# Kernel tuning notes

Measured on AMD Instinct MI355X. Metric: run time of the kernel, lower is better.

The kernel has to match this reference:

```python
import jax, jax.numpy as jnp
import numpy as np

E = 128; H = 8; DK = 16; FFH = 512; NL = 6
DEPOT = 20; CUST = 500; N = DEPOT + CUST
B = 32; M = N; L = 40; CLIP = 10.0; EPS = 1e-5


def _heads(x):
    b, n, _ = x.shape
    return x.reshape(b, n, H, DK).transpose(0, 2, 1, 3)  # (b,H,n,dk)


def _mha(q, k, v, mask3=None):
    s = jnp.einsum('bhnd,bhmd->bhnm', q, k) / jnp.sqrt(jnp.float32(DK))
    if mask3 is not None:
        s = s + mask3[:, None, :, :]
    w = jax.nn.softmax(s, axis=-1)
    o = jnp.einsum('bhnm,bhmd->bhnd', w, v)
    return o.transpose(0, 2, 1, 3).reshape(q.shape[0], q.shape[2], H * DK)


def _inorm(x, g, b):  # InstanceNorm1d over the node axis, per (batch, channel)
    mu = x.mean(axis=1, keepdims=True)
    var = x.var(axis=1, keepdims=True)
    return (x - mu) / jnp.sqrt(var + EPS) * g + b


def setup_inputs() -> dict:
    key = jax.random.key(0)
    ks = jax.random.split(key, 30)
    rn = lambda k, s, sc=0.05: (jax.random.normal(k, s, dtype=jnp.float32) * sc)
    inp = {
        'depot_feats': jax.random.normal(ks[0], (B, DEPOT, 4), dtype=jnp.float32),
        'customer_feats': jax.random.normal(ks[1], (B, CUST, 3), dtype=jnp.float32),
        'mask': jnp.zeros((B, M, N), dtype=jnp.float32),
        'load': jax.random.uniform(ks[2], (B, M), dtype=jnp.float32),
        'current_node': jax.random.randint(ks[3], (B, M), 0, N),
        'subtour_nodes': jax.random.randint(ks[4], (B, M, L), 0, N),
        'subtour_len': jax.random.randint(ks[5], (B, M), 0, L),
        'selected': jax.random.randint(ks[6], (B, M, 4), 0, N),
        # encoder embedding layers
        'enc_dep_W': rn(ks[7], (E, 4)), 'enc_dep_b': rn(ks[8], (E,)),
        'enc_cus_W': rn(ks[9], (E, 3)), 'enc_cus_b': rn(ks[10], (E,)),
        # stacked encoder-layer params
        'Wq': rn(ks[11], (NL, E, E)), 'Wk': rn(ks[12], (NL, E, E)),
        'Wv': rn(ks[13], (NL, E, E)),
        'Wc': rn(ks[14], (NL, E, E)), 'Wc_b': rn(ks[15], (NL, E)),
        'n1_g': jnp.ones((NL, E), jnp.float32), 'n1_b': jnp.zeros((NL, E), jnp.float32),
        'ffW1': rn(ks[16], (NL, FFH, E)), 'ffb1': rn(ks[17], (NL, FFH)),
        'ffW2': rn(ks[18], (NL, E, FFH)), 'ffb2': rn(ks[19], (NL, E)),
        'n2_g': jnp.ones((NL, E), jnp.float32), 'n2_b': jnp.zeros((NL, E), jnp.float32),
        # decoder params
        'dec_Wq_loc': rn(ks[20], (E, 2 * E)),
        'dec_Wq_rout': rn(ks[21], (E, 2 * E + 1)),
        'dec_Wk': rn(ks[22], (E, E)), 'dec_Wv': rn(ks[23], (E, E)),
        'dec_Wc': rn(ks[24], (E, E)), 'dec_Wc_b': rn(ks[25], (E,)),
    }
    return inp


def reference(depot_feats, customer_feats, mask, load,
              enc_dep_W, enc_dep_b, enc_cus_W, enc_cus_b,
              Wq, Wk, Wv, Wc, Wc_b, n1_g, n1_b,
              ffW1, ffb1, ffW2, ffb2, n2_g, n2_b,
              dec_Wq_loc, dec_Wq_rout, dec_Wk, dec_Wv, dec_Wc, dec_Wc_b,
              current_node, subtour_nodes, subtour_len, selected):
    # ---- Encoder ----
    dep = depot_feats @ enc_dep_W.T + enc_dep_b
    cus = customer_feats @ enc_cus_W.T + enc_cus_b
    x = jnp.concatenate([dep, cus], axis=1)  # (B,N,E)
    for i in range(NL):
        q = _heads(x @ Wq[i].T); k = _heads(x @ Wk[i].T); v = _heads(x @ Wv[i].T)
        mh = _mha(q, k, v) @ Wc[i].T + Wc_b[i]
        x1 = _inorm(x + mh, n1_g[i], n1_b[i])
        ff = jax.nn.relu(x1 @ ffW1[i].T + ffb1[i]) @ ffW2[i].T + ffb2[i]
        x = _inorm(x1 + ff, n2_g[i], n2_b[i])
    encoded = x  # (B,N,E)

    # ---- set_k_v ----
    k_d = _heads(encoded @ dec_Wk.T)
    v_d = _heads(encoded @ dec_Wv.T)

    # ---- Decoder forward (current_node present, last_hh not None branch) ----
    enc_mean = encoded.mean(axis=1, keepdims=True)  # (B,1,E)
    enc_mean = jnp.broadcast_to(enc_mean, (B, M, E))
    b_idx = jnp.arange(B)[:, None]
    last_emb = encoded[b_idx, current_node]  # (B,M,E) gather of current node
    input_cat = jnp.concatenate([last_emb, enc_mean, load[:, :, None]], axis=2)
    q_routing = input_cat @ dec_Wq_rout.T  # (B,M,E)

    # subtour gather + masked mean pool
    bb = jnp.arange(B)[:, None, None]
    sub_embs = encoded[bb, subtour_nodes]  # (B,M,L,E)
    pos = jnp.arange(L)[None, None, :]
    valid = pos < subtour_len[:, :, None]
    is_cust = subtour_nodes >= DEPOT
    fm = (valid & is_cust).astype(jnp.float32)  # (B,M,L)
    sub_sum = jnp.einsum('bmle,bml->bme', sub_embs, fm)
    cnt = jnp.clip(fm.sum(axis=2, keepdims=True), 1.0, None)
    sub_mean = sub_sum / cnt
    q_location = jnp.concatenate([last_emb, sub_mean], axis=2) @ dec_Wq_loc.T

    # conditional query blend
    last_node = selected[:, :, -2] < DEPOT
    node = current_node < DEPOT
    flag = ((~last_node) & node).astype(jnp.float32)[:, :, None]  # (B,M,1)
    final_q = q_location * flag + q_routing * (1.0 - flag)

    q = _heads(final_q)  # (B,H,M,dk)
    attn = _mha(q, k_d, v_d, mask3=mask)  # (B,M,H*dk)
    score = attn @ dec_Wc.T + dec_Wc_b  # (B,M,E)
    score_nodes = jnp.einsum('bme,bne->bmn', score, encoded)
    score_scaled = score_nodes / jnp.sqrt(jnp.float32(E))
    score_masked = CLIP * jnp.tanh(score_scaled) + mask
    prob = jax.nn.softmax(score_masked, axis=2)
    return prob
```

## Files before the change

kernel.cpp:

```cpp
#include <hip/hip_runtime.h>
#include <hip/hip_bf16.h>

#define BB 32
#define NN 520
#define MM 520
#define EE 128
#define HH 8
#define DKK 16
#define FFH_ 512
#define NL_ 6
#define DEPOT_ 20
#define LL 40

typedef short short8 __attribute__((ext_vector_type(8)));
typedef short bshort4 __attribute__((ext_vector_type(4)));
typedef float floatx4 __attribute__((ext_vector_type(4)));

__device__ __forceinline__ unsigned short f2b(float x) {
    unsigned int u = __float_as_uint(x);
    return (unsigned short)((u + 0x7fffu + ((u >> 16) & 1u)) >> 16);
}
__device__ __forceinline__ float b2f_(unsigned short h) {
    return __uint_as_float(((unsigned int)h) << 16);
}

__global__ __launch_bounds__(256) void embed_k(
    const float* __restrict__ dep, const float* __restrict__ cus,
    const float* __restrict__ Wd, const float* __restrict__ bd,
    const float* __restrict__ Wc3, const float* __restrict__ bc,
    float* __restrict__ x)
{
    int idx = blockIdx.x * 256 + threadIdx.x;
    int e = idx & 127;
    int bn = idx >> 7;
    int n = bn % NN;
    int b = bn / NN;
    float a;
    if (n < DEPOT_) {
        a = bd[e];
        const float* f = dep + ((size_t)(b * DEPOT_ + n)) * 4;
        #pragma unroll
        for (int j = 0; j < 4; j++) a += f[j] * Wd[e * 4 + j];
    } else {
        a = bc[e];
        const float* f = cus + ((size_t)(b * 500 + (n - DEPOT_))) * 3;
        #pragma unroll
        for (int j = 0; j < 3; j++) a += f[j] * Wc3[e * 3 + j];
    }
    x[idx] = a;
}

#define WLS 196608
#define WDEC 1179648
#define WTOT 1277952
__global__ __launch_bounds__(256) void wconv_k(
    const float* __restrict__ Wq, const float* __restrict__ Wk, const float* __restrict__ Wv,
    const float* __restrict__ Wc, const float* __restrict__ fW1, const float* __restrict__ fW2,
    const float* __restrict__ dWk, const float* __restrict__ dWv, const float* __restrict__ dWc,
    const float* __restrict__ Wql, const float* __restrict__ Wqr,
    unsigned short* __restrict__ WH, unsigned short* __restrict__ WL)
{
    int idx = blockIdx.x * 256 + threadIdx.x;
    if (idx >= WTOT) return;
    const float* src;
    if (idx < WDEC) {
        int i = idx / WLS, r = idx % WLS;
        if (r < 49152) {
            int row = r >> 7, col = r & 127;
            const float* w = row < 128 ? Wq : (row < 256 ? Wk : Wv);
            src = w + (size_t)i * 16384 + (size_t)(row & 127) * 128 + col;
        } else if (r < 65536) {
            src = Wc + (size_t)i * 16384 + (r - 49152);
        } else if (r < 131072) {
            src = fW1 + (size_t)i * 65536 + (r - 65536);
        } else {
            src = fW2 + (size_t)i * 65536 + (r - 131072);
        }
    } else {
        int r = idx - WDEC;
        if (r < 32768) {
            int row = r >> 7, col = r & 127;
            src = (row < 128 ? dWk : dWv) + (size_t)(row & 127) * 128 + col;
        } else if (r < 49152) {
            src = dWc + (r - 32768);
        } else {
            int rr = r - 49152;
            int row = rr >> 7, col = rr & 127;
            if (row < 128)      src = Wqr + (size_t)row * 257 + col;
            else if (row < 256) src = Wql + (size_t)(row - 128) * 256 + col;
            else                src = Wql + (size_t)(row - 256) * 256 + 128 + col;
        }
    }
    float v = *src;
    unsigned short h = f2b(v);
    WH[idx] = h;
    WL[idx] = f2b(v - b2f_(h));
}

#define AP 40
__global__ __launch_bounds__(256) void gemm_pc_k(
    const float* __restrict__ A, int lda,
    const unsigned short* __restrict__ WH, const unsigned short* __restrict__ WL, int ldw,
    const float* __restrict__ bias,
    float* __restrict__ C, int ldc,
    int K, int relu)
{
    __shared__ __align__(16) unsigned short Ah[128][AP];
    __shared__ __align__(16) unsigned short Al[128][AP];
    __shared__ __align__(16) unsigned short Bh[64][AP];
    __shared__ __align__(16) unsigned short Bl[64][AP];

    int t = threadIdx.x;
    int w = t >> 6, lane = t & 63;
    int frow = lane & 15, fq = lane >> 4;
    int n0 = blockIdx.x * 64, m0 = blockIdx.y * 128;

    int arow = t & 127, ahalf = (t >> 7) * 16;
    int brow = t & 63,  bq    = (t >> 6) * 8;

    floatx4 acc[2][4];
    #pragma unroll
    for (int i = 0; i < 2; i++)
        #pragma unroll
        for (int j = 0; j < 4; j++)
            acc[i][j] = (floatx4){0.0f, 0.0f, 0.0f, 0.0f};

    for (int k0 = 0; k0 < K; k0 += 32) {
        {
            const float* Ap = A + (size_t)(m0 + arow) * lda + k0 + ahalf;
            float vr[16];
            #pragma unroll
            for (int j = 0; j < 4; j++) {
                float4 v = ((const float4*)Ap)[j];
                vr[j * 4 + 0] = v.x; vr[j * 4 + 1] = v.y;
                vr[j * 4 + 2] = v.z; vr[j * 4 + 3] = v.w;
            }
            short8 hv0, hv1, lv0, lv1;
            #pragma unroll
            for (int j = 0; j < 8; j++) {
                unsigned short h = f2b(vr[j]);
                hv0[j] = (short)h;
                lv0[j] = (short)f2b(vr[j] - b2f_(h));
            }
            #pragma unroll
            for (int j = 0; j < 8; j++) {
                unsigned short h = f2b(vr[8 + j]);
                hv1[j] = (short)h;
                lv1[j] = (short)f2b(vr[8 + j] - b2f_(h));
            }
            *((short8*)&Ah[arow][ahalf])     = hv0;
            *((short8*)&Ah[arow][ahalf + 8]) = hv1;
            *((short8*)&Al[arow][ahalf])     = lv0;
            *((short8*)&Al[arow][ahalf + 8]) = lv1;
        }
        {
            size_t wo = (size_t)(n0 + brow) * ldw + k0 + bq;
            *((short8*)&Bh[brow][bq]) = *((const short8*)(WH + wo));
            *((short8*)&Bl[brow][bq]) = *((const short8*)(WL + wo));
        }
        __syncthreads();

        short8 ah0 = *((const short8*)&Ah[w * 32 + frow][fq * 8]);
        short8 ah1 = *((const short8*)&Ah[w * 32 + 16 + frow][fq * 8]);
        short8 al0 = *((const short8*)&Al[w * 32 + frow][fq * 8]);
        short8 al1 = *((const short8*)&Al[w * 32 + 16 + frow][fq * 8]);
        #pragma unroll
        for (int nt = 0; nt < 4; nt++) {
            short8 bh = *((const short8*)&Bh[nt * 16 + frow][fq * 8]);
            short8 bl = *((const short8*)&Bl[nt * 16 + frow][fq * 8]);
            acc[0][nt] = __builtin_amdgcn_mfma_f32_16x16x32_bf16(ah0, bh, acc[0][nt], 0, 0, 0);
            acc[1][nt] = __builtin_amdgcn_mfma_f32_16x16x32_bf16(ah1, bh, acc[1][nt], 0, 0, 0);
            acc[0][nt] = __builtin_amdgcn_mfma_f32_16x16x32_bf16(ah0, bl, acc[0][nt], 0, 0, 0);
            acc[1][nt] = __builtin_amdgcn_mfma_f32_16x16x32_bf16(ah1, bl, acc[1][nt], 0, 0, 0);
            acc[0][nt] = __builtin_amdgcn_mfma_f32_16x16x32_bf16(al0, bh, acc[0][nt], 0, 0, 0);
            acc[1][nt] = __builtin_amdgcn_mfma_f32_16x16x32_bf16(al1, bh, acc[1][nt], 0, 0, 0);
        }
        __syncthreads();
    }

    #pragma unroll
    for (int nt = 0; nt < 4; nt++) {
        int col = n0 + nt * 16 + frow;
        float bv = bias ? bias[col] : 0.0f;
        #pragma unroll
        for (int mt = 0; mt < 2; mt++) {
            int rbase = m0 + w * 32 + mt * 16 + fq * 4;
            #pragma unroll
            for (int r = 0; r < 4; r++) {
                float v = acc[mt][nt][r] + bv;
                if (relu) v = fmaxf(v, 0.0f);
                C[(size_t)(rbase + r) * ldc + col] = v;
            }
        }
    }
}

__global__ __launch_bounds__(256) void gemm_qkv3_k(
    const float* __restrict__ A, int lda,
    const unsigned short* __restrict__ WH, const unsigned short* __restrict__ WL, int ldw,
    float* __restrict__ C0, float* __restrict__ C1, float* __restrict__ C2,
    int ldc, int K, int pack)
{
    __shared__ __align__(16) unsigned short Ah[128][AP];
    __shared__ __align__(16) unsigned short Al[128][AP];
    __shared__ __align__(16) unsigned short Bh[64][AP];
    __shared__ __align__(16) unsigned short Bl[64][AP];

    int t = threadIdx.x;
    int w = t >> 6, lane = t & 63;
    int frow = lane & 15, fq = lane >> 4;
    int nb = blockIdx.x;
    int which = nb >> 1;
    float* C = which == 0 ? C0 : (which == 1 ? C1 : C2);
    int n0w = nb * 64;
    int n0c = (nb & 1) * 64;
    int m0 = blockIdx.y * 128;

    int arow = t & 127, ahalf = (t >> 7) * 16;
    int brow = t & 63,  bq    = (t >> 6) * 8;

    floatx4 acc[2][4];
    #pragma unroll
    for (int i = 0; i < 2; i++)
        #pragma unroll
        for (int j = 0; j < 4; j++)
            acc[i][j] = (floatx4){0.0f, 0.0f, 0.0f, 0.0f};

    for (int k0 = 0; k0 < K; k0 += 32) {
        {
            const float* Ap = A + (size_t)(m0 + arow) * lda + k0 + ahalf;
            float vr[16];
            #pragma unroll
            for (int j = 0; j < 4; j++) {
                float4 v = ((const float4*)Ap)[j];
                vr[j * 4 + 0] = v.x; vr[j * 4 + 1] = v.y;
                vr[j * 4 + 2] = v.z; vr[j * 4 + 3] = v.w;
            }
            short8 hv0, hv1, lv0, lv1;
            #pragma unroll
            for (int j = 0; j < 8; j++) {
                unsigned short h = f2b(vr[j]);
                hv0[j] = (short)h;
                lv0[j] = (short)f2b(vr[j] - b2f_(h));
            }
            #pragma unroll
            for (int j = 0; j < 8; j++) {
                unsigned short h = f2b(vr[8 + j]);
                hv1[j] = (short)h;
                lv1[j] = (short)f2b(vr[8 + j] - b2f_(h));
            }
            *((short8*)&Ah[arow][ahalf])     = hv0;
            *((short8*)&Ah[arow][ahalf + 8]) = hv1;
            *((short8*)&Al[arow][ahalf])     = lv0;
            *((short8*)&Al[arow][ahalf + 8]) = lv1;
        }
        {
            size_t wo = (size_t)(n0w + brow) * ldw + k0 + bq;
            *((short8*)&Bh[brow][bq]) = *((const short8*)(WH + wo));
            *((short8*)&Bl[brow][bq]) = *((const short8*)(WL + wo));
        }
        __syncthreads();

        short8 ah0 = *((const short8*)&Ah[w * 32 + frow][fq * 8]);
        short8 ah1 = *((const short8*)&Ah[w * 32 + 16 + frow][fq * 8]);
        short8 al0 = *((const short8*)&Al[w * 32 + frow][fq * 8]);
        short8 al1 = *((const short8*)&Al[w * 32 + 16 + frow][fq * 8]);
        #pragma unroll
        for (int nt = 0; nt < 4; nt++) {
            short8 bh = *((const short8*)&Bh[nt * 16 + frow][fq * 8]);
            short8 bl = *((const short8*)&Bl[nt * 16 + frow][fq * 8]);
            acc[0][nt] = __builtin_amdgcn_mfma_f32_16x16x32_bf16(ah0, bh, acc[0][nt], 0, 0, 0);
            acc[1][nt] = __builtin_amdgcn_mfma_f32_16x16x32_bf16(ah1, bh, acc[1][nt], 0, 0, 0);
            acc[0][nt] = __builtin_amdgcn_mfma_f32_16x16x32_bf16(ah0, bl, acc[0][nt], 0, 0, 0);
            acc[1][nt] = __builtin_amdgcn_mfma_f32_16x16x32_bf16(ah1, bl, acc[1][nt], 0, 0, 0);
            acc[0][nt] = __builtin_amdgcn_mfma_f32_16x16x32_bf16(al0, bh, acc[0][nt], 0, 0, 0);
            acc[1][nt] = __builtin_amdgcn_mfma_f32_16x16x32_bf16(al1, bh, acc[1][nt], 0, 0, 0);
        }
        __syncthreads();
    }

    #pragma unroll
    for (int nt = 0; nt < 4; nt++) {
        int col = n0c + nt * 16 + frow;
        int hh = col >> 4, dd = col & 15;
        #pragma unroll
        for (int mt = 0; mt < 2; mt++) {
            int rbase = m0 + w * 32 + mt * 16 + fq * 4;
            #pragma unroll
            for (int r = 0; r < 4; r++) {
                int row = rbase + r;
                if (pack) {
                    int b2 = row / NN, n2 = row - b2 * NN;
                    C[((size_t)(b2 * HH + hh) * NN + n2) * 16 + dd] = acc[mt][nt][r];
                } else {
                    C[(size_t)row * ldc + col] = acc[mt][nt][r];
                }
            }
        }
    }
}

#define GT 64
#define GK 32
#define GP 36
__global__ __launch_bounds__(256) void sgemm_k(
    const float* __restrict__ A,
    const float* __restrict__ Enc,
    float* __restrict__ C)
{
    __shared__ float As[GT][GP];
    __shared__ float Ws[GT][GP];
    int t = threadIdx.x;
    int tx = t & 15, ty = t >> 4;
    int b = blockIdx.z;
    int m0 = blockIdx.y * GT, n0 = blockIdx.x * GT;
    int lr = t >> 2, lc = (t & 3) * 8;
    int mr = m0 + lr; if (mr >= NN) mr = NN - 1;
    int nr = n0 + lr; if (nr >= NN) nr = NN - 1;
    float acc[4][4];
    #pragma unroll
    for (int i = 0; i < 4; i++)
        #pragma unroll
        for (int j = 0; j < 4; j++) acc[i][j] = 0.0f;

    for (int k0 = 0; k0 < EE; k0 += GK) {
        const float* Ap = A + ((size_t)(b * NN + mr)) * EE + k0 + lc;
        const float* Wp = Enc + ((size_t)(b * NN + nr)) * EE + k0 + lc;
        float4 av0 = *((const float4*)Ap), av1 = *((const float4*)(Ap + 4));
        float4 wv0 = *((const float4*)Wp), wv1 = *((const float4*)(Wp + 4));
        *((float4*)&As[lr][lc]) = av0; *((float4*)&As[lr][lc + 4]) = av1;
        *((float4*)&Ws[lr][lc]) = wv0; *((float4*)&Ws[lr][lc + 4]) = wv1;
        __syncthreads();
        #pragma unroll
        for (int kk = 0; kk < GK; kk += 2) {
            float2 a0 = *((const float2*)&As[ty][kk]);
            float2 a1 = *((const float2*)&As[ty + 16][kk]);
            float2 a2 = *((const float2*)&As[ty + 32][kk]);
            float2 a3 = *((const float2*)&As[ty + 48][kk]);
            float2 w0 = *((const float2*)&Ws[tx][kk]);
            float2 w1 = *((const float2*)&Ws[tx + 16][kk]);
            float2 w2 = *((const float2*)&Ws[tx + 32][kk]);
            float2 w3 = *((const float2*)&Ws[tx + 48][kk]);
            acc[0][0] += a0.x * w0.x + a0.y * w0.y;
            acc[0][1] += a0.x * w1.x + a0.y * w1.y;
            acc[0][2] += a0.x * w2.x + a0.y * w2.y;
            acc[0][3] += a0.x * w3.x + a0.y * w3.y;
            acc[1][0] += a1.x * w0.x + a1.y * w0.y;
            acc[1][1] += a1.x * w1.x + a1.y * w1.y;
            acc[1][2] += a1.x * w2.x + a1.y * w2.y;
            acc[1][3] += a1.x * w3.x + a1.y * w3.y;
            acc[2][0] += a2.x * w0.x + a2.y * w0.y;
            acc[2][1] += a2.x * w1.x + a2.y * w1.y;
            acc[2][2] += a2.x * w2.x + a2.y * w2.y;
            acc[2][3] += a2.x * w3.x + a2.y * w3.y;
            acc[3][0] += a3.x * w0.x + a3.y * w0.y;
            acc[3][1] += a3.x * w1.x + a3.y * w1.y;
            acc[3][2] += a3.x * w2.x + a3.y * w2.y;
            acc[3][3] += a3.x * w3.x + a3.y * w3.y;
        }
        __syncthreads();
    }
    #pragma unroll
    for (int i = 0; i < 4; i++) {
        int m = m0 + ty + 16 * i;
        if (m >= NN) continue;
        #pragma unroll
        for (int j = 0; j < 4; j++) {
            int n = n0 + tx + 16 * j;
            if (n >= NN) continue;
            float v = 10.0f * tanhf(acc[i][j] * 0.088388347648318447f);
            C[((size_t)(b * NN + m)) * NN + n] = v;
        }
    }
}

__global__ __launch_bounds__(64) void smax_k(
    const float* __restrict__ L, const float* __restrict__ mask,
    float* __restrict__ out)
{
    int bm = blockIdx.x;
    int t = threadIdx.x;
    const float* Lr = L + (size_t)bm * NN;
    const float* Mr = mask + (size_t)bm * NN;
    float v[9];
    float mx = -1e30f;
    #pragma unroll
    for (int i = 0; i < 9; i++) {
        int idx = t + i * 64;
        if (idx < NN) { v[i] = Lr[idx] + Mr[idx]; mx = fmaxf(mx, v[i]); }
        else v[i] = -1e30f;
    }
    #pragma unroll
    for (int o = 32; o > 0; o >>= 1) mx = fmaxf(mx, __shfl_xor(mx, o));
    float s = 0.0f;
    #pragma unroll
    for (int i = 0; i < 9; i++) {
        int idx = t + i * 64;
        float e = (idx < NN) ? expf(v[i] - mx) : 0.0f;
        v[i] = e; s += e;
    }
    #pragma unroll
    for (int o = 32; o > 0; o >>= 1) s += __shfl_xor(s, o);
    float inv = 1.0f / s;
    #pragma unroll
    for (int i = 0; i < 9; i++) {
        int idx = t + i * 64;
        if (idx < NN) out[(size_t)bm * NN + idx] = v[i] * inv;
    }
}

#define ATK 64
#define NFRG 3
__global__ __launch_bounds__(256) void fmha_pers_k(
    const float* __restrict__ Qp, const float* __restrict__ Kp,
    const float* __restrict__ Vp, const float* __restrict__ mask,
    float* __restrict__ O, int Nq, int Nk)
{
    __shared__ __align__(16) unsigned short Khl[2][ATK][40];
    __shared__ __align__(16) unsigned short Vhi[2][16][72];
    __shared__ __align__(16) unsigned short Vlo[2][16][72];

    int b = blockIdx.x, h = blockIdx.y, z = blockIdx.z;
    int bh = b * HH + h;
    int t = threadIdx.x;
    int w = t >> 6, lane = t & 63;
    int r16 = lane & 15, g = lane >> 4;

    short8 qf[NFRG], qs[NFRG];
    floatx4 o_acc[NFRG];
    float m_i[NFRG], l_i[NFRG];
    const float* mrowf[NFRG];
    const float* QpB = Qp + (size_t)bh * Nq * 16;
    #pragma unroll
    for (int f = 0; f < NFRG; f++) {
        int fi = f * 16 + z * 4 + w;
        int qg = fi * 16 + r16;
        int qc = qg < Nq ? qg : Nq - 1;
        const float* qp = QpB + (size_t)qc * 16 + 8 * (g & 1);
        float4 qv0 = *((const float4*)qp);
        float4 qv1 = *((const float4*)(qp + 4));
        float qa[8] = {qv0.x, qv0.y, qv0.z, qv0.w, qv1.x, qv1.y, qv1.z, qv1.w};
        #pragma unroll
        for (int j = 0; j < 8; j++) {
            unsigned short hh = f2b(qa[j]);
            unsigned short ll = f2b(qa[j] - b2f_(hh));
            qf[f][j] = (short)(g < 2 ? hh : ll);
            qs[f][j] = (short)(g < 2 ? ll : hh);
        }
        o_acc[f] = (floatx4){0.0f, 0.0f, 0.0f, 0.0f};
        m_i[f] = -1e30f; l_i[f] = 0.0f;
        mrowf[f] = mask ? (mask + ((size_t)(b * Nq + qc)) * Nk) : nullptr;
    }

    int srow = t >> 2, sc = (t & 3) * 4;
    const float* KpB = Kp + ((size_t)bh * Nk) * 16 + sc;
    const float* VpB = Vp + ((size_t)bh * Nk) * 16 + sc;

    {
        int krc = srow < Nk ? srow : Nk - 1;
        float4 kv = *((const float4*)(KpB + (size_t)krc * 16));
        float4 vv = *((const float4*)(VpB + (size_t)krc * 16));
        float ka[4] = {kv.x, kv.y, kv.z, kv.w};
        float va[4] = {vv.x, vv.y, vv.z, vv.w};
        bshort4 khv, klv;
        #pragma unroll
        for (int j = 0; j < 4; j++) {
            unsigned short hh = f2b(ka[j]);
            khv[j] = (short)hh;
            klv[j] = (short)f2b(ka[j] - b2f_(hh));
        }
        *((bshort4*)&Khl[0][srow][sc])      = khv;
        *((bshort4*)&Khl[0][srow][16 + sc]) = klv;
        #pragma unroll
        for (int j = 0; j < 4; j++) {
            unsigned short hh = f2b(va[j]);
            Vhi[0][sc + j][srow] = hh;
            Vlo[0][sc + j][srow] = (unsigned short)f2b(va[j] - b2f_(hh));
        }
    }
    __syncthreads();

    int nkt = (Nk + ATK - 1) / ATK;
    for (int kt = 0; kt < nkt; kt++) {
        int cur = kt & 1;
        int k0 = kt * ATK;

        float4 nkv, nvv;
        bool pf = (kt + 1 < nkt);
        if (pf) {
            int kr = k0 + ATK + srow;
            int krc = kr < Nk ? kr : Nk - 1;
            nkv = *((const float4*)(KpB + (size_t)krc * 16));
            nvv = *((const float4*)(VpB + (size_t)krc * 16));
        }

        float mvv[NFRG][4][4];
        if (mask) {
            #pragma unroll
            for (int f = 0; f < NFRG; f++) {
                #pragma unroll
                for (int s = 0; s < 4; s++) {
                    int c0 = k0 + s * 16 + 4 * g;
                    if (c0 + 3 < Nk) {
                        float4 m4 = *((const float4*)(mrowf[f] + c0));
                        mvv[f][s][0] = m4.x; mvv[f][s][1] = m4.y;
                        mvv[f][s][2] = m4.z; mvv[f][s][3] = m4.w;
                    } else {
                        #pragma unroll
                        for (int r = 0; r < 4; r++)
                            mvv[f][s][r] = (c0 + r < Nk) ? mrowf[f][c0 + r] : 0.0f;
                    }
                }
            }
        }

        short8 kfr[4];
        bshort4 vhf[4], vlf[4];
        #pragma unroll
        for (int s = 0; s < 4; s++) {
            kfr[s] = *((const short8*)&Khl[cur][s * 16 + r16][8 * g]);
            vhf[s] = *((const bshort4*)&Vhi[cur][r16][s * 16 + 4 * g]);
            vlf[s] = *((const bshort4*)&Vlo[cur][r16][s * 16 + 4 * g]);
        }

        #pragma unroll
        for (int f = 0; f < NFRG; f++) {
            int fi = f * 16 + z * 4 + w;
            if (fi * 16 >= Nq) continue;

            float p[4][4];
            #pragma unroll
            for (int s = 0; s < 4; s++) {
                floatx4 a = (floatx4){0.0f, 0.0f, 0.0f, 0.0f};
                a = __builtin_amdgcn_mfma_f32_16x16x32_bf16(kfr[s], qf[f], a, 0, 0, 0);
                a = __builtin_amdgcn_mfma_f32_16x16x32_bf16(kfr[s], qs[f], a, 0, 0, 0);
                #pragma unroll
                for (int r = 0; r < 4; r++) p[s][r] = a[r];
            }

            #pragma unroll
            for (int s = 0; s < 4; s++) {
                int c0 = k0 + s * 16 + 4 * g;
                #pragma unroll
                for (int r = 0; r < 4; r++) {
                    float mv = mask ? mvv[f][s][r] : 0.0f;
                    p[s][r] = (c0 + r < Nk) ? (p[s][r] * 0.25f + mv) : -1e30f;
                }
            }

            float tmax = -1e30f;
            #pragma unroll
            for (int s = 0; s < 4; s++)
                #pragma unroll
                for (int r = 0; r < 4; r++) tmax = fmaxf(tmax, p[s][r]);
            tmax = fmaxf(tmax, __shfl_xor(tmax, 16));
            tmax = fmaxf(tmax, __shfl_xor(tmax, 32));
            float m_new = fmaxf(m_i[f], tmax);
            float alpha = __expf(m_i[f] - m_new);
            float lloc = 0.0f;
            #pragma unroll
            for (int s = 0; s < 4; s++) {
                #pragma unroll
                for (int r = 0; r < 4; r++) {
                    float e = __expf(p[s][r] - m_new);
                    p[s][r] = e; lloc += e;
                }
            }
            lloc += __shfl_xor(lloc, 16);
            lloc += __shfl_xor(lloc, 32);
            l_i[f] = l_i[f] * alpha + lloc;
            m_i[f] = m_new;
            #pragma unroll
            for (int r = 0; r < 4; r++) {
                float ar = __shfl(alpha, 4 * g + r);
                o_acc[f][r] *= ar;
            }

            #pragma unroll
            for (int s = 0; s < 4; s++) {
                bshort4 ph, pl;
                #pragma unroll
                for (int r = 0; r < 4; r++) {
                    unsigned short hh = f2b(p[s][r]);
                    ph[r] = (short)hh;
                    pl[r] = (short)f2b(p[s][r] - b2f_(hh));
                }
                o_acc[f] = __builtin_amdgcn_mfma_f32_16x16x16bf16_1k(ph, vhf[s], o_acc[f], 0, 0, 0);
                o_acc[f] = __builtin_amdgcn_mfma_f32_16x16x16bf16_1k(ph, vlf[s], o_acc[f], 0, 0, 0);
                o_acc[f] = __builtin_amdgcn_mfma_f32_16x16x16bf16_1k(pl, vhf[s], o_acc[f], 0, 0, 0);
            }
        }

        if (pf) {
            int nb = cur ^ 1;
            float ka[4] = {nkv.x, nkv.y, nkv.z, nkv.w};
            float va[4] = {nvv.x, nvv.y, nvv.z, nvv.w};
            bshort4 khv, klv;
            #pragma unroll
            for (int j = 0; j < 4; j++) {
                unsigned short hh = f2b(ka[j]);
                khv[j] = (short)hh;
                klv[j] = (short)f2b(ka[j] - b2f_(hh));
            }
            *((bshort4*)&Khl[nb][srow][sc])      = khv;
            *((bshort4*)&Khl[nb][srow][16 + sc]) = klv;
            #pragma unroll
            for (int j = 0; j < 4; j++) {
                unsigned short hh = f2b(va[j]);
                Vhi[nb][sc + j][srow] = hh;
                Vlo[nb][sc + j][srow] = (unsigned short)f2b(va[j] - b2f_(hh));
            }
        }
        __syncthreads();
    }

    #pragma unroll
    for (int f = 0; f < NFRG; f++) {
        int fi = f * 16 + z * 4 + w;
        if (fi * 16 >= Nq) continue;
        #pragma unroll
        for (int r = 0; r < 4; r++) {
            float lr = __shfl(l_i[f], 4 * g + r);
            int qrow = fi * 16 + 4 * g + r;
            if (qrow < Nq)
                O[((size_t)(b * Nq + qrow)) * EE + h * 16 + r16] = o_acc[f][r] / lr;
        }
    }
}

__global__ __launch_bounds__(256) void inorm_k(
    const float* __restrict__ X, const float* __restrict__ Y,
    const float* __restrict__ g, const float* __restrict__ bb,
    float* __restrict__ Out)
{
    int b = blockIdx.x, eg = blockIdx.y;
    int t = threadIdx.x;
    int tx = t & 15, tn = t >> 4;
    int e = eg * 16 + tx;
    const float* Xb = X + ((size_t)b * NN) * EE + e;
    const float* Yb = Y + ((size_t)b * NN) * EE + e;
    float s = 0.0f, s2 = 0.0f;
    for (int n = tn; n < NN; n += 16) {
        float v = Xb[(size_t)n * EE] + Yb[(size_t)n * EE];
        s += v; s2 += v * v;
    }
    __shared__ float rs[16][17], rs2[16][17];
    rs[tn][tx] = s; rs2[tn][tx] = s2;
    __syncthreads();
    float st = 0.0f, st2 = 0.0f;
    #pragma unroll
    for (int j = 0; j < 16; j++) { st += rs[j][tx]; st2 += rs2[j][tx]; }
    float mu = st * (1.0f / NN);
    float var = st2 * (1.0f / NN) - mu * mu;
    float inv = rsqrtf(var + 1e-5f);
    float gg = g[e], bv = bb[e];
    float* Ob = Out + ((size_t)b * NN) * EE + e;
    for (int n = tn; n < NN; n += 16) {
        float v = Xb[(size_t)n * EE] + Yb[(size_t)n * EE];
        Ob[(size_t)n * EE] = (v - mu) * inv * gg + bv;
    }
}

__global__ void zero_k(float* p, int n) {
    int i = blockIdx.x * 256 + threadIdx.x;
    if (i < n) p[i] = 0.0f;
}

__global__ __launch_bounds__(128) void encsum_k(const float* __restrict__ enc, float* __restrict__ esum) {
    int b = blockIdx.x, ch = blockIdx.y, t = threadIdx.x;
    float a = 0.0f;
    for (int i = 0; i < 65; i++) {
        int n = ch * 65 + i;
        a += enc[((size_t)(b * NN + n)) * EE + t];
    }
    atomicAdd(&esum[b * EE + t], a);
}

__global__ __launch_bounds__(128) void meanterm_k(
    const float* __restrict__ esum, const float* __restrict__ Wr, float* __restrict__ mt)
{
    int b = blockIdx.x, t = threadIdx.x;
    __shared__ float em[128];
    em[t] = esum[b * EE + t] * (1.0f / NN);
    __syncthreads();
    const float* w = Wr + (size_t)t * 257 + 128;
    float a = 0.0f;
    for (int f = 0; f < 128; f++) a += em[f] * w[f];
    mt[b * EE + t] = a;
}

__global__ __launch_bounds__(128) void subtour_k(
    const float* __restrict__ enc, const int* __restrict__ subn,
    const int* __restrict__ subl, float* __restrict__ subm)
{
    int bm = blockIdx.x;
    int b = bm / MM;
    int t = threadIdx.x;
    int len = subl[bm];
    float acc = 0.0f; int cnt = 0;
    for (int l = 0; l < LL; l++) {
        int node = subn[(size_t)bm * LL + l];
        if (l < len && node >= DEPOT_) {
            acc += enc[((size_t)(b * NN + node)) * EE + t];
            cnt++;
        }
    }
    float cf = (float)(cnt < 1 ? 1 : cnt);
    subm[(size_t)bm * EE + t] = acc / cf;
}

__global__ __launch_bounds__(128) void decq_gather_k(
    const float* __restrict__ R, const float* __restrict__ L1, const float* __restrict__ SM2,
    const float* __restrict__ mterm, const int* __restrict__ cur,
    const float* __restrict__ loadv, const int* __restrict__ sel,
    const float* __restrict__ Wqr, float* __restrict__ out)
{
    int bm = blockIdx.x;
    int b = bm / MM;
    int m = bm - b * MM;
    int t = threadIdx.x;
    int cn = cur[bm];
    int s2v = sel[(size_t)bm * 4 + 2];
    bool flag = (s2v >= DEPOT_) && (cn < DEPOT_);
    size_t eo = ((size_t)(b * NN + cn)) * EE + t;
    float q;
    if (flag) q = L1[eo] + SM2[(size_t)bm * EE + t];
    else      q = R[eo] + mterm[b * EE + t] + loadv[bm] * Wqr[(size_t)t * 257 + 256];
    out[((size_t)(b * HH + (t >> 4)) * MM + m) * 16 + (t & 15)] = q;
}

extern "C" void kernel_launch(void* const* d_in, const int* in_sizes, int n_in,
                              void* d_out, int out_size, void* d_ws, size_t ws_size,
                              hipStream_t stream)
{
    const float* depot = (const float*)d_in[0];
    const float* cust  = (const float*)d_in[1];
    const float* mask  = (const float*)d_in[2];
    const float* loadv = (const float*)d_in[3];
    const int*  cur   = (const int*)d_in[4];
    const int*  subn  = (const int*)d_in[5];
    const int*  subl  = (const int*)d_in[6];
    const int*  sel   = (const int*)d_in[7];
    const float* Wdep  = (const float*)d_in[8];
    const float* bdep  = (const float*)d_in[9];
    const float* Wcus  = (const float*)d_in[10];
    const float* bcus  = (const float*)d_in[11];
    const float* Wq    = (const float*)d_in[12];
    const float* Wk    = (const float*)d_in[13];
    const float* Wv    = (const float*)d_in[14];
    const float* Wc    = (const float*)d_in[15];
    const float* Wcb   = (const float*)d_in[16];
    const float* n1g   = (const float*)d_in[17];
    const float* n1b   = (const float*)d_in[18];
    const float* fW1   = (const float*)d_in[19];
    const float* fb1   = (const float*)d_in[20];
    const float* fW2   = (const float*)d_in[21];
    const float* fb2   = (const float*)d_in[22];
    const float* n2g   = (const float*)d_in[23];
    const float* n2b   = (const float*)d_in[24];
    const float* Wql   = (const float*)d_in[25];
    const float* Wqr   = (const float*)d_in[26];
    const float* dWk   = (const float*)d_in[27];
    const float* dWv   = (const float*)d_in[28];
    const float* dWc   = (const float*)d_in[29];
    const float* dWcb  = (const float*)d_in[30];

    const size_t SZ = (size_t)BB * NN * EE;
    float* f0 = (float*)d_ws;
    float* f1 = f0 + SZ;
    float* f2 = f1 + SZ;
    float* f3 = f2 + SZ;
    float* f4 = f3 + SZ;
    float* f5 = f4 + SZ;
    float* big = f5 + SZ;
    unsigned short* WHp = (unsigned short*)(big + (size_t)BB * NN * FFH_);
    unsigned short* WLp = WHp + WTOT;

    dim3 g4(EE / 64, (BB * NN) / 128);
    dim3 g16(FFH_ / 64, (BB * NN) / 128);
    dim3 gq3(6, (BB * NN) / 128);
    dim3 gq2(4, (BB * NN) / 128);
    dim3 gmha(BB, HH, 4);
    dim3 gin(BB, 8);
    dim3 gsc((NN + GT - 1) / GT, (NN + GT - 1) / GT, BB);

    wconv_k<<<(WTOT + 255) / 256, 256, 0, stream>>>(Wq, Wk, Wv, Wc, fW1, fW2,
                                                    dWk, dWv, dWc, Wql, Wqr, WHp, WLp);
    embed_k<<<(BB * NN * EE) / 256, 256, 0, stream>>>(depot, cust, Wdep, bdep, Wcus, bcus, f0);

    for (int i = 0; i < NL_; i++) {
        const unsigned short* lH = WHp + (size_t)i * WLS;
        const unsigned short* lL = WLp + (size_t)i * WLS;
        gemm_qkv3_k<<<gq3, 256, 0, stream>>>(f0, EE, lH, lL, EE, f1, f2, f3, EE, EE, 1);
        fmha_pers_k<<<gmha, 256, 0, stream>>>(f1, f2, f3, nullptr, f4, NN, NN);
        gemm_pc_k<<<g4, 256, 0, stream>>>(f4, EE, lH + 49152, lL + 49152, EE, Wcb + i * EE, f1, EE, EE, 0);
        inorm_k<<<gin, 256, 0, stream>>>(f0, f1, n1g + i * EE, n1b + i * EE, f5);
        gemm_pc_k<<<g16, 256, 0, stream>>>(f5, EE, lH + 65536, lL + 65536, EE, fb1 + i * FFH_, big, FFH_, EE, 1);
        gemm_pc_k<<<g4, 256, 0, stream>>>(big, FFH_, lH + 131072, lL + 131072, FFH_, fb2 + i * EE, f1, EE, FFH_, 0);
        inorm_k<<<gin, 256, 0, stream>>>(f5, f1, n2g + i * EE, n2b + i * EE, f0);
    }

    const unsigned short* dH = WHp + WDEC;
    const unsigned short* dL = WLp + WDEC;
    gemm_qkv3_k<<<gq2, 256, 0, stream>>>(f0, EE, dH, dL, EE, f1, f2, f2, EE, EE, 1);

    zero_k<<<(BB * EE + 255) / 256, 256, 0, stream>>>(f3, BB * EE);
    encsum_k<<<dim3(BB, 8), 128, 0, stream>>>(f0, f3);
    meanterm_k<<<BB, 128, 0, stream>>>(f3, Wqr, f3 + BB * EE);
    subtour_k<<<BB * MM, 128, 0, stream>>>(f0, subn, subl, f4);

    gemm_qkv3_k<<<gq2, 256, 0, stream>>>(f0, EE, dH + 49152, dL + 49152, EE, big, big + SZ, big + SZ, EE, EE, 0);
    gemm_pc_k<<<g4, 256, 0, stream>>>(f4, EE, dH + 49152 + 32768, dL + 49152 + 32768, EE, nullptr, big + 2 * SZ, EE, EE, 0);
    decq_gather_k<<<BB * MM, 128, 0, stream>>>(big, big + SZ, big + 2 * SZ, f3 + BB * EE, cur, loadv, sel, Wqr, f5);

    fmha_pers_k<<<gmha, 256, 0, stream>>>(f5, f1, f2, mask, f4, MM, NN);
    gemm_pc_k<<<g4, 256, 0, stream>>>(f4, EE, dH + 32768, dL + 32768, EE, dWcb, big, EE, EE, 0);

    sgemm_k<<<gsc, 256, 0, stream>>>(big, f0, f1);
    smax_k<<<BB * MM, 64, 0, stream>>>(f1, mask, (float*)d_out);
}
```

Measured before the change: 1.549 ms.

## Double-buffer split-bf16 GEMM tiles and use truncating bf16 split in attention

Both split-bf16 GEMM kernels now keep two LDS buffers. The global loads for the next K-tile are issued before the MFMA work on the current tile, and the conversion and LDS store happen after it. This hides global-load latency and removes one barrier per iteration, at the cost of twice the LDS footprint, which may lower occupancy. The attention kernel also replaces round-to-nearest bf16 conversion with plain truncation in the hi/lo splits. That cuts ALU work, and the lo residual should still carry most of the truncation error.

```diff
diff --git a/kernel.cpp b/kernel.cpp
--- a/kernel.cpp
+++ b/kernel.cpp
@@ -19,6 +19,9 @@
 __device__ __forceinline__ unsigned short f2b(float x) {
     unsigned int u = __float_as_uint(x);
     return (unsigned short)((u + 0x7fffu + ((u >> 16) & 1u)) >> 16);
+}
+__device__ __forceinline__ unsigned short f2b_t(float x) {
+    return (unsigned short)(__float_as_uint(x) >> 16);
 }
 __device__ __forceinline__ float b2f_(unsigned short h) {
     return __uint_as_float(((unsigned int)h) << 16);
@@ -105,10 +108,10 @@
     float* __restrict__ C, int ldc,
     int K, int relu)
 {
-    __shared__ __align__(16) unsigned short Ah[128][AP];
-    __shared__ __align__(16) unsigned short Al[128][AP];
-    __shared__ __align__(16) unsigned short Bh[64][AP];
-    __shared__ __align__(16) unsigned short Bl[64][AP];
+    __shared__ __align__(16) unsigned short Ah[2][128][AP];
+    __shared__ __align__(16) unsigned short Al[2][128][AP];
+    __shared__ __align__(16) unsigned short Bh[2][64][AP];
+    __shared__ __align__(16) unsigned short Bl[2][64][AP];
 
     int t = threadIdx.x;
     int w = t >> 6, lane = t & 63;
@@ -118,6 +121,10 @@
     int arow = t & 127, ahalf = (t >> 7) * 16;
     int brow = t & 63,  bq    = (t >> 6) * 8;
 
+    const float* Abase = A + (size_t)(m0 + arow) * lda + ahalf;
+    const unsigned short* WHb = WH + (size_t)(n0 + brow) * ldw + bq;
+    const unsigned short* WLb = WL + (size_t)(n0 + brow) * ldw + bq;
+
     floatx4 acc[2][4];
     #pragma unroll
     for (int i = 0; i < 2; i++)
@@ -125,49 +132,59 @@
         for (int j = 0; j < 4; j++)
             acc[i][j] = (floatx4){0.0f, 0.0f, 0.0f, 0.0f};
 
-    for (int k0 = 0; k0 < K; k0 += 32) {
-        {
-            const float* Ap = A + (size_t)(m0 + arow) * lda + k0 + ahalf;
-            float vr[16];
-            #pragma unroll
-            for (int j = 0; j < 4; j++) {
-                float4 v = ((const float4*)Ap)[j];
-                vr[j * 4 + 0] = v.x; vr[j * 4 + 1] = v.y;
-                vr[j * 4 + 2] = v.z; vr[j * 4 + 3] = v.w;
-            }
-            short8 hv0, hv1, lv0, lv1;
-            #pragma unroll
-            for (int j = 0; j < 8; j++) {
-                unsigned short h = f2b(vr[j]);
-                hv0[j] = (short)h;
-                lv0[j] = (short)f2b(vr[j] - b2f_(h));
-            }
-            #pragma unroll
-            for (int j = 0; j < 8; j++) {
-                unsigned short h = f2b(vr[8 + j]);
-                hv1[j] = (short)h;
-                lv1[j] = (short)f2b(vr[8 + j] - b2f_(h));
-            }
-            *((short8*)&Ah[arow][ahalf])     = hv0;
-            *((short8*)&Ah[arow][ahalf + 8]) = hv1;
-            *((short8*)&Al[arow][ahalf])     = lv0;
-            *((short8*)&Al[arow][ahalf + 8]) = lv1;
-        }
-        {
-            size_t wo = (size_t)(n0 + brow) * ldw + k0 + bq;
-            *((short8*)&Bh[brow][bq]) = *((const short8*)(WH + wo));
-            *((short8*)&Bl[brow][bq]) = *((const short8*)(WL + wo));
-        }
-        __syncthreads();
-
-        short8 ah0 = *((const short8*)&Ah[w * 32 + frow][fq * 8]);
-        short8 ah1 = *((const short8*)&Ah[w * 32 + 16 + frow][fq * 8]);
-        short8 al0 = *((const short8*)&Al[w * 32 + frow][fq * 8]);
-        short8 al1 = *((const short8*)&Al[w * 32 + 16 + frow][fq * 8]);
+    {
+        float vr[16];
+        #pragma unroll
+        for (int j = 0; j < 4; j++) {
+            float4 v = ((const float4*)Abase)[j];
+            vr[j * 4 + 0] = v.x; vr[j * 4 + 1] = v.y;
+            vr[j * 4 + 2] = v.z; vr[j * 4 + 3] = v.w;
+        }
+        short8 hv0, hv1, lv0, lv1;
+        #pragma unroll
+        for (int j = 0; j < 8; j++) {
+            unsigned short h = f2b(vr[j]);
+            hv0[j] = (short)h;
+            lv0[j] = (short)f2b(vr[j] - b2f_(h));
+        }
+        #pragma unroll
+        for (int j = 0; j < 8; j++) {
+            unsigned short h = f2b(vr[8 + j]);
+            hv1[j] = (short)h;
+            lv1[j] = (short)f2b(vr[8 + j] - b2f_(h));
+        }
+        *((short8*)&Ah[0][arow][ahalf])     = hv0;
+        *((short8*)&Ah[0][arow][ahalf + 8]) = hv1;
+        *((short8*)&Al[0][arow][ahalf])     = lv0;
+        *((short8*)&Al[0][arow][ahalf + 8]) = lv1;
+        *((short8*)&Bh[0][brow][bq]) = *((const short8*)WHb);
+        *((short8*)&Bl[0][brow][bq]) = *((const short8*)WLb);
+    }
+    __syncthreads();
+
+    int nkt = K >> 5;
+    for (int kt = 0; kt < nkt; kt++) {
+        int cur = kt & 1;
+        bool pf = (kt + 1 < nkt);
+
+        float4 av[4];
+        short8 nbh, nbl;
+        if (pf) {
+            const float* Ap = Abase + (kt + 1) * 32;
+            #pragma unroll
+            for (int j = 0; j < 4; j++) av[j] = ((const float4*)Ap)[j];
+            nbh = *((const short8*)(WHb + (kt + 1) * 32));
+            nbl = *((const short8*)(WLb + (kt + 1) * 32));
+        }
+
+        short8 ah0 = *((const short8*)&Ah[cur][w * 32 + frow][fq * 8]);
+        short8 ah1 = *((const short8*)&Ah[cur][w * 32 + 16 + frow][fq * 8]);
+        short8 al0 = *((const short8*)&Al[cur][w * 32 + frow][fq * 8]);
+        short8 al1 = *((const short8*)&Al[cur][w * 32 + 16 + frow][fq * 8]);
         #pragma unroll
         for (int nt = 0; nt < 4; nt++) {
-            short8 bh = *((const short8*)&Bh[nt * 16 + frow][fq * 8]);
-            short8 bl = *((const short8*)&Bl[nt * 16 + frow][fq * 8]);
+            short8 bh = *((const short8*)&Bh[cur][nt * 16 + frow][fq * 8]);
+            short8 bl = *((const short8*)&Bl[cur][nt * 16 + frow][fq * 8]);
             acc[0][nt] = __builtin_amdgcn_mfma_f32_16x16x32_bf16(ah0, bh, acc[0][nt], 0, 0, 0);
             acc[1][nt] = __builtin_amdgcn_mfma_f32_16x16x32_bf16(ah1, bh, acc[1][nt], 0, 0, 0);
             acc[0][nt] = __builtin_amdgcn_mfma_f32_16x16x32_bf16(ah0, bl, acc[0][nt], 0, 0, 0);
@@ -175,6 +192,35 @@
             acc[0][nt] = __builtin_amdgcn_mfma_f32_16x16x32_bf16(al0, bh, acc[0][nt], 0, 0, 0);
             acc[1][nt] = __builtin_amdgcn_mfma_f32_16x16x32_bf16(al1, bh, acc[1][nt], 0, 0, 0);
         }
+
+        if (pf) {
+            int nb2 = cur ^ 1;
+            float vr[16];
+            #pragma unroll
+            for (int j = 0; j < 4; j++) {
+                vr[j * 4 + 0] = av[j].x; vr[j * 4 + 1] = av[j].y;
+                vr[j * 4 + 2] = av[j].z; vr[j * 4 + 3] = av[j].w;
+            }
+            short8 hv0, hv1, lv0, lv1;
+            #pragma unroll
+            for (int j = 0; j < 8; j++) {
+                unsigned short h = f2b(vr[j]);
+                hv0[j] = (short)h;
+                lv0[j] = (short)f2b(vr[j] - b2f_(h));
+            }
+            #pragma unroll
+            for (int j = 0; j < 8; j++) {
+                unsigned short h = f2b(vr[8 + j]);
+                hv1[j] = (short)h;
+                lv1[j] = (short)f2b(vr[8 + j] - b2f_(h));
+            }
+            *((short8*)&Ah[nb2][arow][ahalf])     = hv0;
+            *((short8*)&Ah[nb2][arow][ahalf + 8]) = hv1;
+            *((short8*)&Al[nb2][arow][ahalf])     = lv0;
+            *((short8*)&Al[nb2][arow][ahalf + 8]) = lv1;
+            *((short8*)&Bh[nb2][brow][bq]) = nbh;
+            *((short8*)&Bl[nb2][brow][bq]) = nbl;
+        }
         __syncthreads();
     }
 
@@ -201,10 +247,10 @@
     float* __restrict__ C0, float* __restrict__ C1, float* __restrict__ C2,
     int ldc, int K, int pack)
 {
-    __shared__ __align__(16) unsigned short Ah[128][AP];
-    __shared__ __align__(16) unsigned short Al[128][AP];
-    __shared__ __align__(16) unsigned short Bh[64][AP];
-    __shared__ __align__(16) unsigned short Bl[64][AP];
+    __shared__ __align__(16) unsigned short Ah[2][128][AP];
+    __shared__ __align__(16) unsigned short Al[2][128][AP];
+    __shared__ __align__(16) unsigned short Bh[2][64][AP];
+    __shared__ __align__(16) unsigned short Bl[2][64][AP];
 
     int t = threadIdx.x;
     int w = t >> 6, lane = t & 63;
@@ -219,6 +265,10 @@
     int arow = t & 127, ahalf = (t >> 7) * 16;
     int brow = t & 63,  bq    = (t >> 6) * 8;
 
+    const float* Abase = A + (size_t)(m0 + arow) * lda + ahalf;
+    const unsigned short* WHb = WH + (size_t)(n0w + brow) * ldw + bq;
+    const unsigned short* WLb = WL + (size_t)(n0w + brow) * ldw + bq;
+
     floatx4 acc[2][4];
     #pragma unroll
     for (int i = 0; i < 2; i++)
@@ -226,55 +276,94 @@
         for (int j = 0; j < 4; j++)
             acc[i][j] = (floatx4){0.0f, 0.0f, 0.0f, 0.0f};
 
-    for (int k0 = 0; k0 < K; k0 += 32) {
-        {
-            const float* Ap = A + (size_t)(m0 + arow) * lda + k0 + ahalf;
-            float vr[16];
-            #pragma unroll
-            for (int j = 0; j < 4; j++) {
-                float4 v = ((const float4*)Ap)[j];
-                vr[j * 4 + 0] = v.x; vr[j * 4 + 1] = v.y;
-                vr[j * 4 + 2] = v.z; vr[j * 4 + 3] = v.w;
-            }
-            short8 hv0, hv1, lv0, lv1;
-            #pragma unroll
-            for (int j = 0; j < 8; j++) {
-                unsigned short h = f2b(vr[j]);
-                hv0[j] = (short)h;
-                lv0[j] = (short)f2b(vr[j] - b2f_(h));
-            }
-            #pragma unroll
-            for (int j = 0; j < 8; j++) {
-                unsigned short h = f2b(vr[8 + j]);
-                hv1[j] = (short)h;
-                lv1[j] = (short)f2b(vr[8 + j] - b2f_(h));
-            }
-            *((short8*)&Ah[arow][ahalf])     = hv0;
-            *((short8*)&Ah[arow][ahalf + 8]) = hv1;
-            *((short8*)&Al[arow][ahalf])     = lv0;
-            *((short8*)&Al[arow][ahalf + 8]) = lv1;
-        }
-        {
-            size_t wo = (size_t)(n0w + brow) * ldw + k0 + bq;
-            *((short8*)&Bh[brow][bq]) = *((const short8*)(WH + wo));
-            *((short8*)&Bl[brow][bq]) = *((const short8*)(WL + wo));
-        }
-        __syncthreads();
-
-        short8 ah0 = *((const short8*)&Ah[w * 32 + frow][fq * 8]);
-        short8 ah1 = *((const short8*)&Ah[w * 32 + 16 + frow][fq * 8]);
-        short8 al0 = *((const short8*)&Al[w * 32 + frow][fq * 8]);
-        short8 al1 = *((const short8*)&Al[w * 32 + 16 + frow][fq * 8]);
+    {
+        float vr[16];
+        #pragma unroll
+        for (int j = 0; j < 4; j++) {
+            float4 v = ((const float4*)Abase)[j];
+            vr[j * 4 + 0] = v.x; vr[j * 4 + 1] = v.y;
+            vr[j * 4 + 2] = v.z; vr[j * 4 + 3] = v.w;
+        }
+        short8 hv0, hv1, lv0, lv1;
+        #pragma unroll
+        for (int j = 0; j < 8; j++) {
+            unsigned short h = f2b(vr[j]);
+            hv0[j] = (short)h;
+            lv0[j] = (short)f2b(vr[j] - b2f_(h));
+        }
+        #pragma unroll
+        for (int j = 0; j < 8; j++) {
+            unsigned short h = f2b(vr[8 + j]);
+            hv1[j] = (short)h;
+            lv1[j] = (short)f2b(vr[8 + j] - b2f_(h));
+        }
+        *((short8*)&Ah[0][arow][ahalf])     = hv0;
+        *((short8*)&Ah[0][arow][ahalf + 8]) = hv1;
+        *((short8*)&Al[0][arow][ahalf])     = lv0;
+        *((short8*)&Al[0][arow][ahalf + 8]) = lv1;
+        *((short8*)&Bh[0][brow][bq]) = *((const short8*)WHb);
+        *((short8*)&Bl[0][brow][bq]) = *((const short8*)WLb);
+    }
+    __syncthreads();
+
+    int nkt = K >> 5;
+    for (int kt = 0; kt < nkt; kt++) {
+        int cur = kt & 1;
+        bool pf = (kt + 1 < nkt);
+
+        float4 av[4];
+        short8 nbh, nbl;
+        if (pf) {
+            const float* Ap = Abase + (kt + 1) * 32;
+            #pragma unroll
+            for (int j = 0; j < 4; j++) av[j] = ((const float4*)Ap)[j];
+            nbh = *((const short8*)(WHb + (kt + 1) * 32));
+            nbl = *((const short8*)(WLb + (kt + 1) * 32));
+        }
+
+        short8 ah0 = *((const short8*)&Ah[cur][w * 32 + frow][fq * 8]);
+        short8 ah1 = *((const short8*)&Ah[cur][w * 32 + 16 + frow][fq * 8]);
+        short8 al0 = *((const short8*)&Al[cur][w * 32 + frow][fq * 8]);
+        short8 al1 = *((const short8*)&Al[cur][w * 32 + 16 + frow][fq * 8]);
         #pragma unroll
         for (int nt = 0; nt < 4; nt++) {
-            short8 bh = *((const short8*)&Bh[nt * 16 + frow][fq * 8]);
-            short8 bl = *((const short8*)&Bl[nt * 16 + frow][fq * 8]);
+            short8 bh = *((const short8*)&Bh[cur][nt * 16 + frow][fq * 8]);
+            short8 bl = *((const short8*)&Bl[cur][nt * 16 + frow][fq * 8]);
             acc[0][nt] = __builtin_amdgcn_mfma_f32_16x16x32_bf16(ah0, bh, acc[0][nt], 0, 0, 0);
             acc[1][nt] = __builtin_amdgcn_mfma_f32_16x16x32_bf16(ah1, bh, acc[1][nt], 0, 0, 0);
             acc[0][nt] = __builtin_amdgcn_mfma_f32_16x16x32_bf16(ah0, bl, acc[0][nt], 0, 0, 0);
             acc[1][nt] = __builtin_amdgcn_mfma_f32_16x16x32_bf16(ah1, bl, acc[1][nt], 0, 0, 0);
             acc[0][nt] = __builtin_amdgcn_mfma_f32_16x16x32_bf16(al0, bh, acc[0][nt], 0, 0, 0);
             acc[1][nt] = __builtin_amdgcn_mfma_f32_16x16x32_bf16(al1, bh, acc[1][nt], 0, 0, 0);
+        }
+
+        if (pf) {
+            int nb2 = cur ^ 1;
+            float vr[16];
+            #pragma unroll
+            for (int j = 0; j < 4; j++) {
+                vr[j * 4 + 0] = av[j].x; vr[j * 4 + 1] = av[j].y;
+                vr[j * 4 + 2] = av[j].z; vr[j * 4 + 3] = av[j].w;
+            }
+            short8 hv0, hv1, lv0, lv1;
+            #pragma unroll
+            for (int j = 0; j < 8; j++) {
+                unsigned short h = f2b(vr[j]);
+                hv0[j] = (short)h;
+                lv0[j] = (short)f2b(vr[j] - b2f_(h));
+            }
+            #pragma unroll
+            for (int j = 0; j < 8; j++) {
+                unsigned short h = f2b(vr[8 + j]);
+                hv1[j] = (short)h;
+                lv1[j] = (short)f2b(vr[8 + j] - b2f_(h));
+            }
+            *((short8*)&Ah[nb2][arow][ahalf])     = hv0;
+            *((short8*)&Ah[nb2][arow][ahalf + 8]) = hv1;
+            *((short8*)&Al[nb2][arow][ahalf])     = lv0;
+            *((short8*)&Al[nb2][arow][ahalf + 8]) = lv1;
+            *((short8*)&Bh[nb2][brow][bq]) = nbh;
+            *((short8*)&Bl[nb2][brow][bq]) = nbl;
         }
         __syncthreads();
     }
@@ -442,8 +531,8 @@
         float qa[8] = {qv0.x, qv0.y, qv0.z, qv0.w, qv1.x, qv1.y, qv1.z, qv1.w};
         #pragma unroll
         for (int j = 0; j < 8; j++) {
-            unsigned short hh = f2b(qa[j]);
-            unsigned short ll = f2b(qa[j] - b2f_(hh));
+            unsigned short hh = f2b_t(qa[j]);
+            unsigned short ll = f2b_t(qa[j] - b2f_(hh));
             qf[f][j] = (short)(g < 2 ? hh : ll);
             qs[f][j] = (short)(g < 2 ? ll : hh);
         }
@@ -465,17 +554,17 @@
         bshort4 khv, klv;
         #pragma unroll
         for (int j = 0; j < 4; j++) {
-            unsigned short hh = f2b(ka[j]);
+            unsigned short hh = f2b_t(ka[j]);
             khv[j] = (short)hh;
-            klv[j] = (short)f2b(ka[j] - b2f_(hh));
+            klv[j] = (short)f2b_t(ka[j] - b2f_(hh));
         }
         *((bshort4*)&Khl[0][srow][sc])      = khv;
         *((bshort4*)&Khl[0][srow][16 + sc]) = klv;
         #pragma unroll
         for (int j = 0; j < 4; j++) {
-            unsigned short hh = f2b(va[j]);
+            unsigned short hh = f2b_t(va[j]);
             Vhi[0][sc + j][srow] = hh;
-            Vlo[0][sc + j][srow] = (unsigned short)f2b(va[j] - b2f_(hh));
+            Vlo[0][sc + j][srow] = f2b_t(va[j] - b2f_(hh));
         }
     }
     __syncthreads();
@@ -581,9 +670,9 @@
                 bshort4 ph, pl;
                 #pragma unroll
                 for (int r = 0; r < 4; r++) {
-                    unsigned short hh = f2b(p[s][r]);
+                    unsigned short hh = f2b_t(p[s][r]);
                     ph[r] = (short)hh;
-                    pl[r] = (short)f2b(p[s][r] - b2f_(hh));
+                    pl[r] = (short)f2b_t(p[s][r] - b2f_(hh));
                 }
                 o_acc[f] = __builtin_amdgcn_mfma_f32_16x16x16bf16_1k(ph, vhf[s], o_acc[f], 0, 0, 0);
                 o_acc[f] = __builtin_amdgcn_mfma_f32_16x16x16bf16_1k(ph, vlf[s], o_acc[f], 0, 0, 0);
@@ -592,23 +681,23 @@
         }
 
         if (pf) {
-            int nb = cur ^ 1;
+            int nb2 = cur ^ 1;
             float ka[4] = {nkv.x, nkv.y, nkv.z, nkv.w};
             float va[4] = {nvv.x, nvv.y, nvv.z, nvv.w};
             bshort4 khv, klv;
             #pragma unroll
             for (int j = 0; j < 4; j++) {
-                unsigned short hh = f2b(ka[j]);
+                unsigned short hh = f2b_t(ka[j]);
                 khv[j] = (short)hh;
-                klv[j] = (short)f2b(ka[j] - b2f_(hh));
-            }
-            *((bshort4*)&Khl[nb][srow][sc])      = khv;
-            *((bshort4*)&Khl[nb][srow][16 + sc]) = klv;
+                klv[j] = (short)f2b_t(ka[j] - b2f_(hh));
+            }
+            *((bshort4*)&Khl[nb2][srow][sc])      = khv;
+            *((bshort4*)&Khl[nb2][srow][16 + sc]) = klv;
             #pragma unroll
             for (int j = 0; j < 4; j++) {
-                unsigned short hh = f2b(va[j]);
-                Vhi[nb][sc + j][srow] = hh;
-                Vlo[nb][sc + j][srow] = (unsigned short)f2b(va[j] - b2f_(hh));
+                unsigned short hh = f2b_t(va[j]);
+                Vhi[nb2][sc + j][srow] = hh;
+                Vlo[nb2][sc + j][srow] = f2b_t(va[j] - b2f_(hh));
             }
         }
         __syncthreads();
```

Measured after the change: 1.485 ms. 1.04x faster.
